# Kernel tuning notes

Hardware: AMD Instinct MI355X
Metric: run time of the kernel (lower is better)

## Reference

```python
import jax, jax.numpy as jnp
import numpy as np

NUM_CLASS = 3
LIMIT = 576.0 * 576.0   # from __init__ default limit=576*576
EPS = 1e-5              # normalize_with_limit eps
COS_EPS = 1e-8          # cosine_similarity eps
BIG = 1e9               # 'infinity' for EDT init (>> max possible squared dist)


def _edt(mask):
    """Exact Euclidean distance transform of a binary [H,W] mask.
    For nonzero pixels: distance to nearest zero pixel (scipy semantics).
    Separable squared EDT via brute-force min-plus 1D transforms."""
    H, W = mask.shape
    f = jnp.where(mask > 0, jnp.float32(BIG), jnp.float32(0.0))  # [H,W] sq dists
    jw = jnp.arange(W, dtype=jnp.float32)
    r2w = (jw[:, None] - jw[None, :]) ** 2  # [W,W] (j-k)^2
    jh = jnp.arange(H, dtype=jnp.float32)
    r2h = (jh[:, None] - jh[None, :]) ** 2  # [H,H]
    # pass along width: d[i,j] = min_k f[i,k] + (j-k)^2
    d = jnp.min(f[:, None, :] + r2w[None, :, :], axis=-1)        # [H,W]
    # pass along height: d[i,j] = min_k d[k,j] + (i-k)^2
    d = jnp.min(d.T[:, None, :] + r2h[None, :, :], axis=-1).T    # [H,W]
    return jnp.sqrt(d)


def _norm_limit(x):
    m = jnp.minimum(jnp.max(x), jnp.float32(LIMIT))
    return x / (m + jnp.float32(EPS))


def _dw(mask):
    return _norm_limit(_edt(mask))


def setup_inputs() -> dict:
    key = jax.random.key(0)
    k1, k2 = jax.random.split(key)
    B, C, H, W = 4, NUM_CLASS, 256, 256
    pred = jax.random.normal(k1, (B, C, H, W), dtype=jnp.float32)
    lab = jax.random.randint(k2, (B, H, W), 0, C, dtype=jnp.int32)
    return {"pred": pred, "lab": lab}


def reference(pred, lab):
    B, C, H, W = pred.shape
    pred_lbl = jnp.argmax(pred, axis=1)              # [B,H,W]
    lab = lab.reshape(pred_lbl.shape)

    lab_oh = jax.nn.one_hot(lab, C, dtype=jnp.float32)        # [B,H,W,C]
    pred_oh = jax.nn.one_hot(pred_lbl, C, dtype=jnp.float32)  # [B,H,W,C]
    lab_oh_c = jnp.moveaxis(lab_oh, -1, 1)           # [B,C,H,W] == getBAV masks
    pred_oh_c = jnp.moveaxis(pred_oh, -1, 1)

    # per-class distance weights (normalized EDT) -- sequential map keeps memory low
    lab_dw = jax.lax.map(_dw, lab_oh_c.reshape(B * C, H, W)).reshape(B, C, H, W)
    pred_dw = jax.lax.map(_dw, pred_oh_c.reshape(B * C, H, W)).reshape(B, C, H, W)

    # feat = [sum_c dw ; one_hot] -> [B, 1+C, H, W]
    lab_feat = jnp.concatenate([jnp.sum(lab_dw, axis=1, keepdims=True), lab_oh_c], axis=1)
    pred_feat = jnp.concatenate([jnp.sum(pred_dw, axis=1, keepdims=True), pred_oh_c], axis=1)

    # cosine similarity per pixel over the (1+C)=4 channel dim
    dot = jnp.sum(pred_feat * lab_feat, axis=1)                # [B,H,W]
    na = jnp.sqrt(jnp.sum(pred_feat * pred_feat, axis=1))
    nb = jnp.sqrt(jnp.sum(lab_feat * lab_feat, axis=1))
    sim = dot / (jnp.maximum(na, COS_EPS) * jnp.maximum(nb, COS_EPS))

    loss_b = 1.0 - jnp.mean(sim.reshape(B, -1), axis=1)        # [B]
    has_fg = jnp.sum((lab > 0).astype(jnp.int32), axis=(1, 2)) > 0
    loss = jnp.sum(jnp.where(has_fg, loss_b, 0.0)) / B
    return jnp.nan_to_num(loss, nan=0.0, posinf=1.0, neginf=0.0)
```

## Files before the change

### kernel.cpp

```cpp
#include <hip/hip_runtime.h>
#include <hip/hip_bf16.h>

#define HH 256
#define WW 256
#define BB 4
#define CC 3
#define HW 65536
#define NM 24
#define BIGF 1e9f
#define LIMITF 331776.0f
#define EPSF 1e-5f


__global__ __launch_bounds__(256) void k_rowpass(const float* __restrict__ pred,
                                                 const int* __restrict__ lab,
                                                 float* __restrict__ dbuf,
                                                 unsigned char* __restrict__ codes) {
    int blk = blockIdx.x;
    int b = blk >> 8;
    int i = blk & 255;
    int j = threadIdx.x;

    int lv = lab[(b << 16) + (i << 8) + j];
    const float* pb = pred + (((size_t)(b * 3)) << 16) + (i << 8) + j;
    float p0 = pb[0];
    float p1 = pb[(size_t)1 << 16];
    float p2 = pb[(size_t)2 << 16];
    int am = 0; float v = p0;
    if (p1 > v) { am = 1; v = p1; }
    if (p2 > v) { am = 2; }

    codes[(b << 16) + (i << 8) + j] = (unsigned char)(lv | (am << 2));

    __shared__ unsigned long long zm[6][4];
    int w = threadIdx.x >> 6;
    #pragma unroll
    for (int c = 0; c < 3; ++c) {
        unsigned long long zl = __ballot(lv != c);
        unsigned long long zp = __ballot(am != c);
        if ((threadIdx.x & 63) == 0) { zm[c][w] = zl; zm[3 + c][w] = zp; }
    }
    __syncthreads();

    #pragma unroll
    for (int t = 0; t < 6; ++t) {
        int bestd = 512;
        #pragma unroll
        for (int w2 = 0; w2 < 4; ++w2) {
            unsigned long long z = zm[t][w2];
            int base = w2 << 6;
            int rel = j - base;
            unsigned long long mle;
            if (rel >= 63)      mle = ~0ULL;
            else if (rel < 0)   mle = 0ULL;
            else                mle = (2ULL << rel) - 1ULL;
            unsigned long long zl = z & mle;
            if (zl) {
                int p = base + 63 - __clzll(zl);
                int d = j - p;
                if (d < bestd) bestd = d;
            }
            unsigned long long zr = z & ~mle;
            if (zr) {
                int p = base + __ffsll(zr) - 1;
                int d = p - j;
                if (d < bestd) bestd = d;
            }
        }
        float d1 = (bestd >= 512) ? BIGF : (float)(bestd * bestd);
        int c = (t < 3) ? t : (t - 3);
        int m = ((t < 3) ? 0 : 12) + b * 3 + c;
        dbuf[(((size_t)m) << 16) + (i << 8) + j] = d1;
    }
}

__global__ __launch_bounds__(256) void k_colpass(float* __restrict__ dbuf,
                                                 float* __restrict__ blkmax) {
    int blk = blockIdx.x;
    int m = blk >> 5;
    int j0 = (blk & 31) << 3;
    __shared__ float tile[320 * 9];
    float* base = dbuf + (((size_t)m) << 16);

    {
        int t = threadIdx.x;
        int gr = t >> 3, gc = t & 7;
        tile[gr * 9 + gc] = BIGF;
        tile[(288 + gr) * 9 + gc] = BIGF;
    }
    #pragma unroll
    for (int it = 0; it < 2; ++it) {
        int f = (it << 8) + threadIdx.x;
        int row = f >> 1, half = f & 1;
        float4 v4 = *(const float4*)(base + (row << 8) + j0 + (half << 2));
        int lb = (row + 32) * 9 + (half << 2);
        tile[lb + 0] = v4.x; tile[lb + 1] = v4.y;
        tile[lb + 2] = v4.z; tile[lb + 3] = v4.w;
    }
    __syncthreads();

    int jj = threadIdx.x & 7;
    int ib = threadIdx.x >> 3;

    float acc[8];
    float dmax = 0.0f;
    #pragma unroll
    for (int r = 0; r < 8; ++r) {
        acc[r] = tile[(ib + (r << 5) + 32) * 9 + jj];
        dmax = fmaxf(dmax, acc[r]);
    }
    #pragma unroll
    for (int off = 32; off; off >>= 1)
        dmax = fmaxf(dmax, __shfl_xor(dmax, off, 64));
    int Rmax = (int)sqrtf(dmax) + 1;
    if (Rmax > 255) Rmax = 255;

    if (Rmax <= 32) {
        for (int o = -Rmax; o <= Rmax; ++o) {
            float o2 = (float)(o * o);
            #pragma unroll
            for (int r = 0; r < 8; ++r)
                acc[r] = fminf(acc[r], o2 + tile[(ib + (r << 5) + 32 + o) * 9 + jj]);
        }
    } else {
        for (int o = -Rmax; o <= Rmax; ++o) {
            #pragma unroll
            for (int r = 0; r < 8; ++r) {
                int i = ib + (r << 5);
                int k = i + o;
                k = (k < 0) ? 0 : ((k > 255) ? 255 : k);
                float dk = (float)(k - i);
                acc[r] = fminf(acc[r], fmaf(dk, dk, tile[(k + 32) * 9 + jj]));
            }
        }
    }

    float lmax = 0.0f;
    #pragma unroll
    for (int r = 0; r < 8; ++r) {
        int i = ib + (r << 5);
        base[(i << 8) + j0 + jj] = acc[r];
        lmax = fmaxf(lmax, acc[r]);
    }

    #pragma unroll
    for (int off = 32; off; off >>= 1)
        lmax = fmaxf(lmax, __shfl_down(lmax, off, 64));
    __shared__ float wmax[4];
    if ((threadIdx.x & 63) == 0) wmax[threadIdx.x >> 6] = lmax;
    __syncthreads();
    if (threadIdx.x == 0)
        blkmax[blk] = fmaxf(fmaxf(wmax[0], wmax[1]), fmaxf(wmax[2], wmax[3]));
}

__global__ __launch_bounds__(256) void k_final(const unsigned char* __restrict__ codes,
                                               const float* __restrict__ dbuf,
                                               const float* __restrict__ blkmax,
                                               float* __restrict__ psum,
                                               int* __restrict__ pfg) {
    __shared__ float inv[NM];
    if (threadIdx.x < NM) {
        const float* bm = blkmax + (threadIdx.x << 5);
        float v = 0.0f;
        #pragma unroll
        for (int s = 0; s < 32; ++s) v = fmaxf(v, bm[s]);
        inv[threadIdx.x] = 1.0f / (fminf(sqrtf(v), LIMITF) + EPSF);
    }
    __syncthreads();

    int b = blockIdx.x >> 8;
    int pix = ((blockIdx.x & 255) << 8) + threadIdx.x;

    int code = codes[(b << 16) + pix];
    int lv = code & 3;
    int am = code >> 2;

    float slab = 0.0f, spred = 0.0f;
    #pragma unroll
    for (int c = 0; c < 3; ++c) {
        int ml = b * 3 + c;
        float dl = dbuf[(((size_t)ml) << 16) + pix];
        slab += sqrtf(dl) * inv[ml];
        float dp = dbuf[(((size_t)(ml + 12)) << 16) + pix];
        spred += sqrtf(dp) * inv[ml + 12];
    }

    float dot = spred * slab + ((am == lv) ? 1.0f : 0.0f);
    float na = sqrtf(spred * spred + 1.0f);
    float nb = sqrtf(slab * slab + 1.0f);
    float sim = dot / (fmaxf(na, 1e-8f) * fmaxf(nb, 1e-8f));

    unsigned long long fg = __ballot(lv > 0);

    #pragma unroll
    for (int off = 32; off; off >>= 1)
        sim += __shfl_down(sim, off, 64);
    __shared__ float wsum[4];
    __shared__ int wfg[4];
    if ((threadIdx.x & 63) == 0) {
        wsum[threadIdx.x >> 6] = sim;
        wfg[threadIdx.x >> 6] = (fg != 0ULL) ? 1 : 0;
    }
    __syncthreads();
    if (threadIdx.x == 0) {
        psum[blockIdx.x] = wsum[0] + wsum[1] + wsum[2] + wsum[3];
        pfg[blockIdx.x] = wfg[0] | wfg[1] | wfg[2] | wfg[3];
    }
}

__global__ __launch_bounds__(256) void k_finalize(const float* __restrict__ psum,
                                                  const int* __restrict__ pfg,
                                                  float* __restrict__ out) {
    int t = threadIdx.x;
    int b = t >> 6, l = t & 63;
    int base = (b << 8) + l;
    float s = psum[base] + psum[base + 64] + psum[base + 128] + psum[base + 192];
    int f = pfg[base] | pfg[base + 64] | pfg[base + 128] | pfg[base + 192];
    #pragma unroll
    for (int off = 32; off; off >>= 1) {
        s += __shfl_down(s, off, 64);
        f |= __shfl_down(f, off, 64);
    }
    __shared__ float bsum[4];
    __shared__ int bfg[4];
    if (l == 0) { bsum[b] = s; bfg[b] = f; }
    __syncthreads();
    if (t == 0) {
        float loss = 0.0f;
        for (int bb = 0; bb < BB; ++bb) {
            float lb = 1.0f - bsum[bb] * (1.0f / (float)HW);
            if (bfg[bb]) loss += lb;
        }
        loss *= (1.0f / (float)BB);
        if (isnan(loss)) loss = 0.0f;
        else if (isinf(loss)) loss = (loss > 0.0f) ? 1.0f : 0.0f;
        out[0] = loss;
    }
}

extern "C" void kernel_launch(void* const* d_in, const int* in_sizes, int n_in,
                              void* d_out, int out_size, void* d_ws, size_t ws_size,
                              hipStream_t stream) {
    const float* pred = (const float*)d_in[0];
    const int*   lab  = (const int*)d_in[1];

    char* wsb = (char*)d_ws;
    float* dbuf   = (float*)wsb;
    size_t off    = (size_t)NM * HW * sizeof(float);
    float* blkmax = (float*)(wsb + off);          off += 768 * sizeof(float);
    float* psum   = (float*)(wsb + off);          off += 1024 * sizeof(float);
    int*   pfg    = (int*)  (wsb + off);          off += 1024 * sizeof(int);
    unsigned char* codes = (unsigned char*)(wsb + off);

    k_rowpass <<<BB * HH,  256, 0, stream>>>(pred, lab, dbuf, codes);
    k_colpass <<<NM * 32,  256, 0, stream>>>(dbuf, blkmax);
    k_final   <<<BB * 256, 256, 0, stream>>>(codes, dbuf, blkmax, psum, pfg);
    k_finalize<<<1,        256, 0, stream>>>(psum, pfg, (float*)d_out);
}
```

Before: 80.76 us.

## Fuse four EDT-loss kernels into one persistent kernel with grid barriers

Merges the row pass, column pass, final similarity and finalize kernels into a single 1024-block launch. Stages are separated by hand-written software grid barriers built from per-block flag arrays and a go flag, and block 0 reduces the partial sums and resets the flags at the end. The aim is to remove three kernel launch gaps and the tail time between kernels. The barriers assume all 1024 blocks are co-resident, which is not guaranteed and would deadlock otherwise. The flags also rely on the workspace starting zeroed, and the spin-waiting adds its own cost.

Result: slower. 197.7 us (+144.8%).

```diff
diff --git a/kernel.cpp b/kernel.cpp
--- a/kernel.cpp
+++ b/kernel.cpp
@@ -1,5 +1,4 @@
 #include <hip/hip_runtime.h>
-#include <hip/hip_bf16.h>
 
 #define HH 256
 #define WW 256
@@ -7,240 +6,301 @@
 #define CC 3
 #define HW 65536
 #define NM 24
+#define NBLK 1024
 #define BIGF 1e9f
 #define LIMITF 331776.0f
 #define EPSF 1e-5f
 
-
-__global__ __launch_bounds__(256) void k_rowpass(const float* __restrict__ pred,
-                                                 const int* __restrict__ lab,
-                                                 float* __restrict__ dbuf,
-                                                 unsigned char* __restrict__ codes) {
-    int blk = blockIdx.x;
-    int b = blk >> 8;
-    int i = blk & 255;
-    int j = threadIdx.x;
-
-    int lv = lab[(b << 16) + (i << 8) + j];
-    const float* pb = pred + (((size_t)(b * 3)) << 16) + (i << 8) + j;
-    float p0 = pb[0];
-    float p1 = pb[(size_t)1 << 16];
-    float p2 = pb[(size_t)2 << 16];
-    int am = 0; float v = p0;
-    if (p1 > v) { am = 1; v = p1; }
-    if (p2 > v) { am = 2; }
-
-    codes[(b << 16) + (i << 8) + j] = (unsigned char)(lv | (am << 2));
-
+#define MAGIC1 0x1B7E55ED
+#define MAGIC2 0x2C8F66EE
+#define MAGIC3 0x3D9A77EF
+
+
+struct GFlags {
+    int arr1[NBLK];
+    int arr2[NBLK];
+    int arr3[NBLK];
+    int go1;
+    int go2;
+};
+
+__device__ __forceinline__ int ldf(const int* p) {
+    return __hip_atomic_load(p, __ATOMIC_RELAXED, __HIP_MEMORY_SCOPE_AGENT);
+}
+__device__ __forceinline__ void stf(int* p, int v) {
+    __hip_atomic_store(p, v, __ATOMIC_RELAXED, __HIP_MEMORY_SCOPE_AGENT);
+}
+
+__device__ __forceinline__ void gbar(int bid, int* arr, int* go, int magic) {
+    __syncthreads();
+    if (threadIdx.x == 0) { __threadfence(); stf(&arr[bid], magic); }
+    if (bid == 0) {
+        int i0 = threadIdx.x << 2;
+        #pragma unroll
+        for (int k = 0; k < 4; ++k)
+            while (ldf(&arr[i0 + k]) != magic) __builtin_amdgcn_s_sleep(2);
+        __syncthreads();
+        if (threadIdx.x == 0) stf(go, magic);
+    }
+    if (threadIdx.x == 0) {
+        while (ldf(go) != magic) __builtin_amdgcn_s_sleep(2);
+        __threadfence();
+    }
+    __syncthreads();
+}
+
+__global__ __launch_bounds__(256, 4) void fused(
+        const float* __restrict__ pred, const int* __restrict__ lab,
+        float* __restrict__ dbuf, float* __restrict__ blkmax,
+        float* __restrict__ psum, int* __restrict__ pfg,
+        unsigned char* __restrict__ codes, GFlags* __restrict__ fl,
+        float* __restrict__ out) {
     __shared__ unsigned long long zm[6][4];
-    int w = threadIdx.x >> 6;
-    #pragma unroll
-    for (int c = 0; c < 3; ++c) {
-        unsigned long long zl = __ballot(lv != c);
-        unsigned long long zp = __ballot(am != c);
-        if ((threadIdx.x & 63) == 0) { zm[c][w] = zl; zm[3 + c][w] = zp; }
-    }
-    __syncthreads();
-
-    #pragma unroll
-    for (int t = 0; t < 6; ++t) {
-        int bestd = 512;
-        #pragma unroll
-        for (int w2 = 0; w2 < 4; ++w2) {
-            unsigned long long z = zm[t][w2];
-            int base = w2 << 6;
-            int rel = j - base;
-            unsigned long long mle;
-            if (rel >= 63)      mle = ~0ULL;
-            else if (rel < 0)   mle = 0ULL;
-            else                mle = (2ULL << rel) - 1ULL;
-            unsigned long long zl = z & mle;
-            if (zl) {
-                int p = base + 63 - __clzll(zl);
-                int d = j - p;
-                if (d < bestd) bestd = d;
+    __shared__ float tile[320 * 9];
+    __shared__ float wmax[4];
+    __shared__ float inv[NM];
+    __shared__ float wsum[4];
+    __shared__ int   wfg[4];
+    __shared__ float bsum[4];
+    __shared__ int   bfg[4];
+
+    const int bid = blockIdx.x;
+
+    {
+        int b = bid >> 8;
+        int i = bid & 255;
+        int j = threadIdx.x;
+
+        int lv = lab[(b << 16) + (i << 8) + j];
+        const float* pb = pred + (((size_t)(b * 3)) << 16) + (i << 8) + j;
+        float p0 = pb[0];
+        float p1 = pb[(size_t)1 << 16];
+        float p2 = pb[(size_t)2 << 16];
+        int am = 0; float v = p0;
+        if (p1 > v) { am = 1; v = p1; }
+        if (p2 > v) { am = 2; }
+
+        codes[(b << 16) + (i << 8) + j] = (unsigned char)(lv | (am << 2));
+
+        int w = threadIdx.x >> 6;
+        #pragma unroll
+        for (int c = 0; c < 3; ++c) {
+            unsigned long long zl = __ballot(lv != c);
+            unsigned long long zp = __ballot(am != c);
+            if ((threadIdx.x & 63) == 0) { zm[c][w] = zl; zm[3 + c][w] = zp; }
+        }
+        __syncthreads();
+
+        #pragma unroll
+        for (int t = 0; t < 6; ++t) {
+            int bestd = 512;
+            #pragma unroll
+            for (int w2 = 0; w2 < 4; ++w2) {
+                unsigned long long z = zm[t][w2];
+                int basew = w2 << 6;
+                int rel = j - basew;
+                unsigned long long mle;
+                if (rel >= 63)      mle = ~0ULL;
+                else if (rel < 0)   mle = 0ULL;
+                else                mle = (2ULL << rel) - 1ULL;
+                unsigned long long zlo = z & mle;
+                if (zlo) {
+                    int p = basew + 63 - __clzll(zlo);
+                    int d = j - p;
+                    if (d < bestd) bestd = d;
+                }
+                unsigned long long zr = z & ~mle;
+                if (zr) {
+                    int p = basew + __ffsll(zr) - 1;
+                    int d = p - j;
+                    if (d < bestd) bestd = d;
+                }
             }
-            unsigned long long zr = z & ~mle;
-            if (zr) {
-                int p = base + __ffsll(zr) - 1;
-                int d = p - j;
-                if (d < bestd) bestd = d;
+            float d1 = (bestd >= 512) ? BIGF : (float)(bestd * bestd);
+            int c = (t < 3) ? t : (t - 3);
+            int m = ((t < 3) ? 0 : 12) + b * 3 + c;
+            dbuf[(((size_t)m) << 16) + (i << 8) + j] = d1;
+        }
+    }
+
+    gbar(bid, fl->arr1, &fl->go1, MAGIC1);
+
+    if (bid < NM * 32) {
+        int m = bid >> 5;
+        int j0 = (bid & 31) << 3;
+        float* base = dbuf + (((size_t)m) << 16);
+
+        {
+            int t = threadIdx.x;
+            int gr = t >> 3, gc = t & 7;
+            tile[gr * 9 + gc] = BIGF;
+            tile[(288 + gr) * 9 + gc] = BIGF;
+        }
+        #pragma unroll
+        for (int it = 0; it < 2; ++it) {
+            int f = (it << 8) + threadIdx.x;
+            int row = f >> 1, half = f & 1;
+            float4 v4 = *(const float4*)(base + (row << 8) + j0 + (half << 2));
+            int lb = (row + 32) * 9 + (half << 2);
+            tile[lb + 0] = v4.x; tile[lb + 1] = v4.y;
+            tile[lb + 2] = v4.z; tile[lb + 3] = v4.w;
+        }
+        __syncthreads();
+
+        int jj = threadIdx.x & 7;
+        int ib = threadIdx.x >> 3;
+
+        float acc[8];
+        float dmax = 0.0f;
+        #pragma unroll
+        for (int r = 0; r < 8; ++r) {
+            acc[r] = tile[(ib + (r << 5) + 32) * 9 + jj];
+            dmax = fmaxf(dmax, acc[r]);
+        }
+        #pragma unroll
+        for (int off = 32; off; off >>= 1)
+            dmax = fmaxf(dmax, __shfl_xor(dmax, off, 64));
+        int Rmax = (int)sqrtf(dmax) + 1;
+        if (Rmax > 255) Rmax = 255;
+
+        if (Rmax <= 32) {
+            for (int o = -Rmax; o <= Rmax; ++o) {
+                float o2 = (float)(o * o);
+                #pragma unroll
+                for (int r = 0; r < 8; ++r)
+                    acc[r] = fminf(acc[r], o2 + tile[(ib + (r << 5) + 32 + o) * 9 + jj]);
             }
-        }
-        float d1 = (bestd >= 512) ? BIGF : (float)(bestd * bestd);
-        int c = (t < 3) ? t : (t - 3);
-        int m = ((t < 3) ? 0 : 12) + b * 3 + c;
-        dbuf[(((size_t)m) << 16) + (i << 8) + j] = d1;
-    }
-}
-
-__global__ __launch_bounds__(256) void k_colpass(float* __restrict__ dbuf,
-                                                 float* __restrict__ blkmax) {
-    int blk = blockIdx.x;
-    int m = blk >> 5;
-    int j0 = (blk & 31) << 3;
-    __shared__ float tile[320 * 9];
-    float* base = dbuf + (((size_t)m) << 16);
+        } else {
+            for (int o = -Rmax; o <= Rmax; ++o) {
+                #pragma unroll
+                for (int r = 0; r < 8; ++r) {
+                    int i = ib + (r << 5);
+                    int k = i + o;
+                    k = (k < 0) ? 0 : ((k > 255) ? 255 : k);
+                    float dk = (float)(k - i);
+                    acc[r] = fminf(acc[r], fmaf(dk, dk, tile[(k + 32) * 9 + jj]));
+                }
+            }
+        }
+
+        float lmax = 0.0f;
+        #pragma unroll
+        for (int r = 0; r < 8; ++r) {
+            int i = ib + (r << 5);
+            base[(i << 8) + j0 + jj] = acc[r];
+            lmax = fmaxf(lmax, acc[r]);
+        }
+        #pragma unroll
+        for (int off = 32; off; off >>= 1)
+            lmax = fmaxf(lmax, __shfl_down(lmax, off, 64));
+        if ((threadIdx.x & 63) == 0) wmax[threadIdx.x >> 6] = lmax;
+        __syncthreads();
+        if (threadIdx.x == 0)
+            blkmax[bid] = fmaxf(fmaxf(wmax[0], wmax[1]), fmaxf(wmax[2], wmax[3]));
+    }
+
+    gbar(bid, fl->arr2, &fl->go2, MAGIC2);
 
     {
+        if (threadIdx.x < NM) {
+            const float* bm = blkmax + (threadIdx.x << 5);
+            float v = 0.0f;
+            #pragma unroll
+            for (int s = 0; s < 32; ++s) v = fmaxf(v, bm[s]);
+            inv[threadIdx.x] = 1.0f / (fminf(sqrtf(v), LIMITF) + EPSF);
+        }
+        __syncthreads();
+
+        int b = bid >> 8;
+        int pix = ((bid & 255) << 8) + threadIdx.x;
+
+        int code = codes[(b << 16) + pix];
+        int lv = code & 3;
+        int am = code >> 2;
+
+        float slab = 0.0f, spred = 0.0f;
+        #pragma unroll
+        for (int c = 0; c < 3; ++c) {
+            int ml = b * 3 + c;
+            float dl = dbuf[(((size_t)ml) << 16) + pix];
+            slab += sqrtf(dl) * inv[ml];
+            float dp = dbuf[(((size_t)(ml + 12)) << 16) + pix];
+            spred += sqrtf(dp) * inv[ml + 12];
+        }
+
+        float dot = spred * slab + ((am == lv) ? 1.0f : 0.0f);
+        float na = sqrtf(spred * spred + 1.0f);
+        float nb = sqrtf(slab * slab + 1.0f);
+        float sim = dot / (fmaxf(na, 1e-8f) * fmaxf(nb, 1e-8f));
+
+        unsigned long long fg = __ballot(lv > 0);
+
+        #pragma unroll
+        for (int off = 32; off; off >>= 1)
+            sim += __shfl_down(sim, off, 64);
+        if ((threadIdx.x & 63) == 0) {
+            wsum[threadIdx.x >> 6] = sim;
+            wfg[threadIdx.x >> 6] = (fg != 0ULL) ? 1 : 0;
+        }
+        __syncthreads();
+        if (threadIdx.x == 0) {
+            psum[bid] = wsum[0] + wsum[1] + wsum[2] + wsum[3];
+            pfg[bid] = wfg[0] | wfg[1] | wfg[2] | wfg[3];
+            __threadfence();
+            stf(&fl->arr3[bid], MAGIC3);
+        }
+    }
+
+    if (bid != 0) return;
+
+    {
+        int i0 = threadIdx.x << 2;
+        #pragma unroll
+        for (int k = 0; k < 4; ++k)
+            while (ldf(&fl->arr3[i0 + k]) != MAGIC3) __builtin_amdgcn_s_sleep(2);
+        __syncthreads();
+        if (threadIdx.x == 0) __threadfence();
+        __syncthreads();
+
         int t = threadIdx.x;
-        int gr = t >> 3, gc = t & 7;
-        tile[gr * 9 + gc] = BIGF;
-        tile[(288 + gr) * 9 + gc] = BIGF;
-    }
-    #pragma unroll
-    for (int it = 0; it < 2; ++it) {
-        int f = (it << 8) + threadIdx.x;
-        int row = f >> 1, half = f & 1;
-        float4 v4 = *(const float4*)(base + (row << 8) + j0 + (half << 2));
-        int lb = (row + 32) * 9 + (half << 2);
-        tile[lb + 0] = v4.x; tile[lb + 1] = v4.y;
-        tile[lb + 2] = v4.z; tile[lb + 3] = v4.w;
-    }
-    __syncthreads();
-
-    int jj = threadIdx.x & 7;
-    int ib = threadIdx.x >> 3;
-
-    float acc[8];
-    float dmax = 0.0f;
-    #pragma unroll
-    for (int r = 0; r < 8; ++r) {
-        acc[r] = tile[(ib + (r << 5) + 32) * 9 + jj];
-        dmax = fmaxf(dmax, acc[r]);
-    }
-    #pragma unroll
-    for (int off = 32; off; off >>= 1)
-        dmax = fmaxf(dmax, __shfl_xor(dmax, off, 64));
-    int Rmax = (int)sqrtf(dmax) + 1;
-    if (Rmax > 255) Rmax = 255;
-
-    if (Rmax <= 32) {
-        for (int o = -Rmax; o <= Rmax; ++o) {
-            float o2 = (float)(o * o);
-            #pragma unroll
-            for (int r = 0; r < 8; ++r)
-                acc[r] = fminf(acc[r], o2 + tile[(ib + (r << 5) + 32 + o) * 9 + jj]);
-        }
-    } else {
-        for (int o = -Rmax; o <= Rmax; ++o) {
-            #pragma unroll
-            for (int r = 0; r < 8; ++r) {
-                int i = ib + (r << 5);
-                int k = i + o;
-                k = (k < 0) ? 0 : ((k > 255) ? 255 : k);
-                float dk = (float)(k - i);
-                acc[r] = fminf(acc[r], fmaf(dk, dk, tile[(k + 32) * 9 + jj]));
+        int b = t >> 6, l = t & 63;
+        int base = (b << 8) + l;
+        float s = psum[base] + psum[base + 64] + psum[base + 128] + psum[base + 192];
+        int f = pfg[base] | pfg[base + 64] | pfg[base + 128] | pfg[base + 192];
+        #pragma unroll
+        for (int off = 32; off; off >>= 1) {
+            s += __shfl_down(s, off, 64);
+            f |= __shfl_down(f, off, 64);
+        }
+        if (l == 0) { bsum[b] = s; bfg[b] = f; }
+        __syncthreads();
+        if (t == 0) {
+            float loss = 0.0f;
+            for (int bb = 0; bb < BB; ++bb) {
+                float lb = 1.0f - bsum[bb] * (1.0f / (float)HW);
+                if (bfg[bb]) loss += lb;
             }
-        }
-    }
-
-    float lmax = 0.0f;
-    #pragma unroll
-    for (int r = 0; r < 8; ++r) {
-        int i = ib + (r << 5);
-        base[(i << 8) + j0 + jj] = acc[r];
-        lmax = fmaxf(lmax, acc[r]);
-    }
-
-    #pragma unroll
-    for (int off = 32; off; off >>= 1)
-        lmax = fmaxf(lmax, __shfl_down(lmax, off, 64));
-    __shared__ float wmax[4];
-    if ((threadIdx.x & 63) == 0) wmax[threadIdx.x >> 6] = lmax;
-    __syncthreads();
-    if (threadIdx.x == 0)
-        blkmax[blk] = fmaxf(fmaxf(wmax[0], wmax[1]), fmaxf(wmax[2], wmax[3]));
-}
-
-__global__ __launch_bounds__(256) void k_final(const unsigned char* __restrict__ codes,
-                                               const float* __restrict__ dbuf,
-                                               const float* __restrict__ blkmax,
-                                               float* __restrict__ psum,
-                                               int* __restrict__ pfg) {
-    __shared__ float inv[NM];
-    if (threadIdx.x < NM) {
-        const float* bm = blkmax + (threadIdx.x << 5);
-        float v = 0.0f;
-        #pragma unroll
-        for (int s = 0; s < 32; ++s) v = fmaxf(v, bm[s]);
-        inv[threadIdx.x] = 1.0f / (fminf(sqrtf(v), LIMITF) + EPSF);
-    }
-    __syncthreads();
-
-    int b = blockIdx.x >> 8;
-    int pix = ((blockIdx.x & 255) << 8) + threadIdx.x;
-
-    int code = codes[(b << 16) + pix];
-    int lv = code & 3;
-    int am = code >> 2;
-
-    float slab = 0.0f, spred = 0.0f;
-    #pragma unroll
-    for (int c = 0; c < 3; ++c) {
-        int ml = b * 3 + c;
-        float dl = dbuf[(((size_t)ml) << 16) + pix];
-        slab += sqrtf(dl) * inv[ml];
-        float dp = dbuf[(((size_t)(ml + 12)) << 16) + pix];
-        spred += sqrtf(dp) * inv[ml + 12];
-    }
-
-    float dot = spred * slab + ((am == lv) ? 1.0f : 0.0f);
-    float na = sqrtf(spred * spred + 1.0f);
-    float nb = sqrtf(slab * slab + 1.0f);
-    float sim = dot / (fmaxf(na, 1e-8f) * fmaxf(nb, 1e-8f));
-
-    unsigned long long fg = __ballot(lv > 0);
-
-    #pragma unroll
-    for (int off = 32; off; off >>= 1)
-        sim += __shfl_down(sim, off, 64);
-    __shared__ float wsum[4];
-    __shared__ int wfg[4];
-    if ((threadIdx.x & 63) == 0) {
-        wsum[threadIdx.x >> 6] = sim;
-        wfg[threadIdx.x >> 6] = (fg != 0ULL) ? 1 : 0;
-    }
-    __syncthreads();
-    if (threadIdx.x == 0) {
-        psum[blockIdx.x] = wsum[0] + wsum[1] + wsum[2] + wsum[3];
-        pfg[blockIdx.x] = wfg[0] | wfg[1] | wfg[2] | wfg[3];
-    }
-}
-
-__global__ __launch_bounds__(256) void k_finalize(const float* __restrict__ psum,
-                                                  const int* __restrict__ pfg,
-                                                  float* __restrict__ out) {
-    int t = threadIdx.x;
-    int b = t >> 6, l = t & 63;
-    int base = (b << 8) + l;
-    float s = psum[base] + psum[base + 64] + psum[base + 128] + psum[base + 192];
-    int f = pfg[base] | pfg[base + 64] | pfg[base + 128] | pfg[base + 192];
-    #pragma unroll
-    for (int off = 32; off; off >>= 1) {
-        s += __shfl_down(s, off, 64);
-        f |= __shfl_down(f, off, 64);
-    }
-    __shared__ float bsum[4];
-    __shared__ int bfg[4];
-    if (l == 0) { bsum[b] = s; bfg[b] = f; }
-    __syncthreads();
-    if (t == 0) {
-        float loss = 0.0f;
-        for (int bb = 0; bb < BB; ++bb) {
-            float lb = 1.0f - bsum[bb] * (1.0f / (float)HW);
-            if (bfg[bb]) loss += lb;
-        }
-        loss *= (1.0f / (float)BB);
-        if (isnan(loss)) loss = 0.0f;
-        else if (isinf(loss)) loss = (loss > 0.0f) ? 1.0f : 0.0f;
-        out[0] = loss;
+            loss *= (1.0f / (float)BB);
+            if (isnan(loss)) loss = 0.0f;
+            else if (isinf(loss)) loss = (loss > 0.0f) ? 1.0f : 0.0f;
+            out[0] = loss;
+        }
+
+        __syncthreads();
+        #pragma unroll
+        for (int k = 0; k < 4; ++k) {
+            fl->arr1[i0 + k] = 0;
+            fl->arr2[i0 + k] = 0;
+            fl->arr3[i0 + k] = 0;
+        }
+        if (t == 0) { fl->go1 = 0; fl->go2 = 0; }
     }
 }
 
 extern "C" void kernel_launch(void* const* d_in, const int* in_sizes, int n_in,
                               void* d_out, int out_size, void* d_ws, size_t ws_size,
                               hipStream_t stream) {
+    (void)in_sizes; (void)n_in; (void)out_size; (void)ws_size;
     const float* pred = (const float*)d_in[0];
     const int*   lab  = (const int*)d_in[1];
 
@@ -251,9 +311,9 @@
     float* psum   = (float*)(wsb + off);          off += 1024 * sizeof(float);
     int*   pfg    = (int*)  (wsb + off);          off += 1024 * sizeof(int);
     unsigned char* codes = (unsigned char*)(wsb + off);
-
-    k_rowpass <<<BB * HH,  256, 0, stream>>>(pred, lab, dbuf, codes);
-    k_colpass <<<NM * 32,  256, 0, stream>>>(dbuf, blkmax);
-    k_final   <<<BB * 256, 256, 0, stream>>>(codes, dbuf, blkmax, psum, pfg);
-    k_finalize<<<1,        256, 0, stream>>>(psum, pfg, (float*)d_out);
-}
+    off += (size_t)BB * HW;
+    GFlags* fl = (GFlags*)(wsb + off);
+
+    fused<<<NBLK, 256, 0, stream>>>(pred, lab, dbuf, blkmax, psum, pfg,
+                                    codes, fl, (float*)d_out);
+}
```

## Pass row zero-bitmasks between passes instead of full float row distances

Applied to the files above, without the earlier changes.

The row pass now writes only the per-row 64-bit zero-location bitmasks (24 masks x 256 rows x 4 words) instead of 24 full float distance planes. The column-pass kernel reloads these bitmasks into shared memory and recomputes the 1D row distances for its 8-column strip straight into its tile before the column min-plus. This removes a large global write and read of the intermediate float buffer. In exchange, the bit-scan work moves into the column kernel, where each block recomputes it for its own columns.

Measured after the change: 74.34 us (median of 2 runs). -7.9%, faster.

```diff
diff --git a/kernel.cpp b/kernel.cpp
--- a/kernel.cpp
+++ b/kernel.cpp
@@ -1,5 +1,4 @@
 #include <hip/hip_runtime.h>
-#include <hip/hip_bf16.h>
 
 #define HH 256
 #define WW 256
@@ -7,6 +6,7 @@
 #define CC 3
 #define HW 65536
 #define NM 24
+#define NBLK 1024
 #define BIGF 1e9f
 #define LIMITF 331776.0f
 #define EPSF 1e-5f
@@ -14,7 +14,7 @@
 
 __global__ __launch_bounds__(256) void k_rowpass(const float* __restrict__ pred,
                                                  const int* __restrict__ lab,
-                                                 float* __restrict__ dbuf,
+                                                 unsigned long long* __restrict__ bits,
                                                  unsigned char* __restrict__ codes) {
     int blk = blockIdx.x;
     int b = blk >> 8;
@@ -42,65 +42,72 @@
     }
     __syncthreads();
 
-    #pragma unroll
-    for (int t = 0; t < 6; ++t) {
+    if (threadIdx.x < 24) {
+        int t = threadIdx.x >> 2;
+        int w2 = threadIdx.x & 3;
+        int c = (t < 3) ? t : (t - 3);
+        int m = ((t < 3) ? 0 : 12) + b * 3 + c;
+        bits[(((size_t)m) << 10) + (i << 2) + w2] = zm[t][w2];
+    }
+}
+
+__global__ __launch_bounds__(256) void k_colpass(const unsigned long long* __restrict__ bits,
+                                                 float* __restrict__ dbuf,
+                                                 float* __restrict__ blkmax) {
+    int blk = blockIdx.x;
+    int m = blk >> 5;
+    int j0 = (blk & 31) << 3;
+    __shared__ float tile[320 * 9];
+    __shared__ unsigned long long zb[256][4];
+    float* base = dbuf + (((size_t)m) << 16);
+
+    {
+        const unsigned long long* bm = bits + (((size_t)m) << 10);
+        int t = threadIdx.x;
+        #pragma unroll
+        for (int k = 0; k < 4; ++k) {
+            int idx = t + (k << 8);
+            zb[idx >> 2][idx & 3] = bm[idx];
+        }
+        int gr = t >> 3, gc = t & 7;
+        tile[gr * 9 + gc] = BIGF;
+        tile[(288 + gr) * 9 + gc] = BIGF;
+    }
+    __syncthreads();
+
+    int jj = threadIdx.x & 7;
+    int ib = threadIdx.x >> 3;
+    int j = j0 + jj;
+
+    #pragma unroll
+    for (int r = 0; r < 8; ++r) {
+        int row = ib + (r << 5);
         int bestd = 512;
         #pragma unroll
         for (int w2 = 0; w2 < 4; ++w2) {
-            unsigned long long z = zm[t][w2];
-            int base = w2 << 6;
-            int rel = j - base;
+            unsigned long long z = zb[row][w2];
+            int basew = w2 << 6;
+            int rel = j - basew;
             unsigned long long mle;
             if (rel >= 63)      mle = ~0ULL;
             else if (rel < 0)   mle = 0ULL;
             else                mle = (2ULL << rel) - 1ULL;
-            unsigned long long zl = z & mle;
-            if (zl) {
-                int p = base + 63 - __clzll(zl);
+            unsigned long long zlo = z & mle;
+            if (zlo) {
+                int p = basew + 63 - __clzll(zlo);
                 int d = j - p;
                 if (d < bestd) bestd = d;
             }
             unsigned long long zr = z & ~mle;
             if (zr) {
-                int p = base + __ffsll(zr) - 1;
+                int p = basew + __ffsll(zr) - 1;
                 int d = p - j;
                 if (d < bestd) bestd = d;
             }
         }
-        float d1 = (bestd >= 512) ? BIGF : (float)(bestd * bestd);
-        int c = (t < 3) ? t : (t - 3);
-        int m = ((t < 3) ? 0 : 12) + b * 3 + c;
-        dbuf[(((size_t)m) << 16) + (i << 8) + j] = d1;
-    }
-}
-
-__global__ __launch_bounds__(256) void k_colpass(float* __restrict__ dbuf,
-                                                 float* __restrict__ blkmax) {
-    int blk = blockIdx.x;
-    int m = blk >> 5;
-    int j0 = (blk & 31) << 3;
-    __shared__ float tile[320 * 9];
-    float* base = dbuf + (((size_t)m) << 16);
-
-    {
-        int t = threadIdx.x;
-        int gr = t >> 3, gc = t & 7;
-        tile[gr * 9 + gc] = BIGF;
-        tile[(288 + gr) * 9 + gc] = BIGF;
-    }
-    #pragma unroll
-    for (int it = 0; it < 2; ++it) {
-        int f = (it << 8) + threadIdx.x;
-        int row = f >> 1, half = f & 1;
-        float4 v4 = *(const float4*)(base + (row << 8) + j0 + (half << 2));
-        int lb = (row + 32) * 9 + (half << 2);
-        tile[lb + 0] = v4.x; tile[lb + 1] = v4.y;
-        tile[lb + 2] = v4.z; tile[lb + 3] = v4.w;
-    }
-    __syncthreads();
-
-    int jj = threadIdx.x & 7;
-    int ib = threadIdx.x >> 3;
+        tile[(row + 32) * 9 + jj] = (bestd >= 512) ? BIGF : (float)(bestd * bestd);
+    }
+    __syncthreads();
 
     float acc[8];
     float dmax = 0.0f;
@@ -241,6 +248,7 @@
 extern "C" void kernel_launch(void* const* d_in, const int* in_sizes, int n_in,
                               void* d_out, int out_size, void* d_ws, size_t ws_size,
                               hipStream_t stream) {
+    (void)in_sizes; (void)n_in; (void)out_size; (void)ws_size;
     const float* pred = (const float*)d_in[0];
     const int*   lab  = (const int*)d_in[1];
 
@@ -251,9 +259,12 @@
     float* psum   = (float*)(wsb + off);          off += 1024 * sizeof(float);
     int*   pfg    = (int*)  (wsb + off);          off += 1024 * sizeof(int);
     unsigned char* codes = (unsigned char*)(wsb + off);
-
-    k_rowpass <<<BB * HH,  256, 0, stream>>>(pred, lab, dbuf, codes);
-    k_colpass <<<NM * 32,  256, 0, stream>>>(dbuf, blkmax);
-    k_final   <<<BB * 256, 256, 0, stream>>>(codes, dbuf, blkmax, psum, pfg);
-    k_finalize<<<1,        256, 0, stream>>>(psum, pfg, (float*)d_out);
-}
+    off += (size_t)BB * HW;
+    off = (off + 255) & ~(size_t)255;
+    unsigned long long* bits = (unsigned long long*)(wsb + off);
+
+    k_rowpass <<<NBLK,    256, 0, stream>>>(pred, lab, bits, codes);
+    k_colpass <<<NM * 32, 256, 0, stream>>>(bits, dbuf, blkmax);
+    k_final   <<<NBLK,    256, 0, stream>>>(codes, dbuf, blkmax, psum, pfg);
+    k_finalize<<<1,       256, 0, stream>>>(psum, pfg, (float*)d_out);
+}
```
